# Kernel optimization log

Hardware: AMD Instinct MI355X
Metric: run time of the kernel (lower is better)

The kernel has to match this reference:

```python
import jax, jax.numpy as jnp
import numpy as np
import math

B, N, D = 4, 16384, 256
M, H = 64, 8
HD = D // H

def setup_inputs() -> dict:
    key = jax.random.key(0)
    ks = jax.random.split(key, 5)
    s = 1.0 / math.sqrt(D)
    return {
        "x": jax.random.normal(ks[0], (B, N, D), dtype=jnp.float32),
        "Ws": jax.random.normal(ks[1], (M, D), dtype=jnp.float32) * s,
        "bs": jnp.zeros((M,), dtype=jnp.float32),
        "Wqkv": jax.random.normal(ks[2], (3 * D, D), dtype=jnp.float32) * s,
        "Wo": jax.random.normal(ks[3], (D, D), dtype=jnp.float32) * s,
        "bo": jnp.zeros((D,), dtype=jnp.float32),
    }

def reference(x, Ws, bs, Wqkv, Wo, bo):
    # slice weights: softmax over N (dim=1), matching the torch code exactly
    logits = jnp.einsum('bnd,md->bnm', x, Ws) + bs          # [B,N,M]
    weights = jax.nn.softmax(logits, axis=1)                # softmax over N
    # pooling: tokens[b,m,d] = sum_n w[b,n,m] * x[b,n,d]
    tokens = jnp.einsum('bnm,bnd->bmd', weights, x)         # [B,M,D]
    # qkv projection (no bias)
    qkv = jnp.einsum('bmd,ed->bme', tokens, Wqkv)           # [B,M,3D]
    qkv = qkv.reshape(B, M, 3, H, HD)
    q = qkv[:, :, 0].transpose(0, 2, 1, 3)                  # [B,H,M,HD]
    k = qkv[:, :, 1].transpose(0, 2, 1, 3)
    v = qkv[:, :, 2].transpose(0, 2, 1, 3)
    scale = 1.0 / math.sqrt(HD)
    attn = jax.nn.softmax(jnp.einsum('bhmd,bhkd->bhmk', q, k) * scale, axis=-1)
    token_out = jnp.einsum('bhmk,bhkd->bhmd', attn, v)      # [B,H,M,HD]
    token_out = token_out.transpose(0, 2, 1, 3).reshape(B, M, D)
    token_out = jnp.einsum('bmd,ed->bme', token_out, Wo) + bo
    # unpooling: out[b,n,d] = sum_m w[b,n,m] * token_out[b,m,d]
    out = jnp.einsum('bnm,bmd->bnd', weights, token_out)    # [B,N,D]
    return out
```

## Files before the change

kernel.cpp:

```cpp
#include <hip/hip_runtime.h>
#include <math.h>

constexpr int B = 4;
constexpr int N = 16384;
constexpr int D = 256;
constexpr int M = 64;
constexpr int H = 8;

typedef __attribute__((ext_vector_type(8))) short short8;
typedef __attribute__((ext_vector_type(4))) float floatx4;

__device__ __forceinline__ float4 ld4(const float* p) {
  return *reinterpret_cast<const float4*>(p);
}
__device__ __forceinline__ void st4(float* p, float a, float b, float c, float d) {
  *reinterpret_cast<float4*>(p) = make_float4(a, b, c, d);
}
__device__ __forceinline__ unsigned short f2bf(float f) {
  unsigned u = __float_as_uint(f);
  unsigned r = (u + 0x7fffu + ((u >> 16) & 1u)) >> 16;
  return (unsigned short)r;
}

#define FMA16(acc, a4, b4)                       \
  do {                                           \
    acc[0][0] = fmaf(a4.x, b4.x, acc[0][0]);     \
    acc[0][1] = fmaf(a4.x, b4.y, acc[0][1]);     \
    acc[0][2] = fmaf(a4.x, b4.z, acc[0][2]);     \
    acc[0][3] = fmaf(a4.x, b4.w, acc[0][3]);     \
    acc[1][0] = fmaf(a4.y, b4.x, acc[1][0]);     \
    acc[1][1] = fmaf(a4.y, b4.y, acc[1][1]);     \
    acc[1][2] = fmaf(a4.y, b4.z, acc[1][2]);     \
    acc[1][3] = fmaf(a4.y, b4.w, acc[1][3]);     \
    acc[2][0] = fmaf(a4.z, b4.x, acc[2][0]);     \
    acc[2][1] = fmaf(a4.z, b4.y, acc[2][1]);     \
    acc[2][2] = fmaf(a4.z, b4.z, acc[2][2]);     \
    acc[2][3] = fmaf(a4.z, b4.w, acc[2][3]);     \
    acc[3][0] = fmaf(a4.w, b4.x, acc[3][0]);     \
    acc[3][1] = fmaf(a4.w, b4.y, acc[3][1]);     \
    acc[3][2] = fmaf(a4.w, b4.z, acc[3][2]);     \
    acc[3][3] = fmaf(a4.w, b4.w, acc[3][3]);     \
  } while (0)

__global__ __launch_bounds__(256) void k1_fused(
    const float* __restrict__ x, const float* __restrict__ Ws,
    const float* __restrict__ bs, unsigned short* __restrict__ xbT,
    unsigned short* __restrict__ En, unsigned short* __restrict__ Et,
    float* __restrict__ denom) {
  __shared__ unsigned short Xt[64][264];
  __shared__ unsigned short Wt[64][264];
  __shared__ unsigned short Es[64][72];
  __shared__ float red[64];
  const int b = blockIdx.y;
  const int n0 = blockIdx.x * 64;
  const int tid = threadIdx.x;
  const int w = tid >> 6, l = tid & 63;

#pragma unroll
  for (int p = 0; p < 16; ++p) {
    const int i = p * 256 + tid;
    const int row = i >> 6;
    const int c4 = (i & 63) * 4;
    float4 v = ld4(&x[((size_t)(b * N + n0 + row)) * D + c4]);
    unsigned u0 = (unsigned)f2bf(v.x) | ((unsigned)f2bf(v.y) << 16);
    unsigned u1 = (unsigned)f2bf(v.z) | ((unsigned)f2bf(v.w) << 16);
    *reinterpret_cast<uint2*>(&Xt[row][c4]) = make_uint2(u0, u1);
    float4 wv = ld4(&Ws[(size_t)row * D + c4]);
    unsigned w0 = (unsigned)f2bf(wv.x) | ((unsigned)f2bf(wv.y) << 16);
    unsigned w1 = (unsigned)f2bf(wv.z) | ((unsigned)f2bf(wv.w) << 16);
    *reinterpret_cast<uint2*>(&Wt[row][c4]) = make_uint2(w0, w1);
  }
  if (tid < 64) red[tid] = 0.0f;
  __syncthreads();

  floatx4 acc[4] = {{0.f, 0.f, 0.f, 0.f},
                    {0.f, 0.f, 0.f, 0.f},
                    {0.f, 0.f, 0.f, 0.f},
                    {0.f, 0.f, 0.f, 0.f}};
  const int ar = w * 16 + (l & 15);
  const int q8 = (l >> 4) * 8;
#pragma unroll
  for (int ks = 0; ks < 8; ++ks) {
    short8 a = *reinterpret_cast<short8*>(&Xt[ar][ks * 32 + q8]);
#pragma unroll
    for (int mt = 0; mt < 4; ++mt) {
      short8 bf = *reinterpret_cast<short8*>(&Wt[mt * 16 + (l & 15)][ks * 32 + q8]);
      acc[mt] = __builtin_amdgcn_mfma_f32_16x16x32_bf16(a, bf, acc[mt], 0, 0, 0);
    }
  }

  {
    const int t = tid;
#pragma unroll
    for (int g = 0; g < 4; ++g) {
      unsigned dw[8];
#pragma unroll
      for (int j = 0; j < 8; ++j) {
        const unsigned lo = Xt[g * 16 + 2 * j][t];
        const unsigned hi = Xt[g * 16 + 2 * j + 1][t];
        dw[j] = lo | (hi << 16);
      }
      const size_t base = ((size_t)(b * D + t)) * N + n0 + g * 16;
      *reinterpret_cast<uint4*>(&xbT[base]) =
          make_uint4(dw[0], dw[1], dw[2], dw[3]);
      *reinterpret_cast<uint4*>(&xbT[base + 8]) =
          make_uint4(dw[4], dw[5], dw[6], dw[7]);
    }
  }

#pragma unroll
  for (int mt = 0; mt < 4; ++mt) {
    const int m = mt * 16 + (l & 15);
    const float bsm = bs[m];
    float s = 0.0f;
#pragma unroll
    for (int r = 0; r < 4; ++r) {
      const int n = w * 16 + (l >> 4) * 4 + r;
      const float e = expf(acc[mt][r] + bsm);
      s += e;
      Es[n][m] = f2bf(e);
    }
    atomicAdd(&red[m], s);
  }
  __syncthreads();
  if (tid < 64) atomicAdd(&denom[b * M + tid], red[tid]);
#pragma unroll
  for (int p = 0; p < 2; ++p) {
    const int g = p * 256 + tid;
    const int n = g >> 3;
    const int m0 = (g & 7) * 8;
    short8 v = *reinterpret_cast<short8*>(&Es[n][m0]);
    *reinterpret_cast<short8*>(&En[((size_t)(b * N + n0 + n)) * M + m0]) = v;
  }
#pragma unroll
  for (int p = 0; p < 2; ++p) {
    const int g = p * 256 + tid;
    const int m = g >> 3;
    const int n8 = (g & 7) * 8;
    unsigned short bu[8];
#pragma unroll
    for (int k = 0; k < 8; ++k) bu[k] = Es[n8 + k][m];
    uint4 pk;
    pk.x = (unsigned)bu[0] | ((unsigned)bu[1] << 16);
    pk.y = (unsigned)bu[2] | ((unsigned)bu[3] << 16);
    pk.z = (unsigned)bu[4] | ((unsigned)bu[5] << 16);
    pk.w = (unsigned)bu[6] | ((unsigned)bu[7] << 16);
    *reinterpret_cast<uint4*>(&Et[((size_t)(b * M + m)) * N + n0 + n8]) = pk;
  }
}

__global__ __launch_bounds__(256) void k2_pool(
    const unsigned short* __restrict__ Et, const unsigned short* __restrict__ xbT,
    float* __restrict__ tokens) {
  __shared__ unsigned short EtS[64][72];
  __shared__ unsigned short XtS[64][72];
  const int dt = blockIdx.x, nc = blockIdx.y, b = blockIdx.z;
  const int d0 = dt * 64;
  const int tid = threadIdx.x;
  const int w = tid >> 6, l = tid & 63;
  floatx4 acc[4] = {{0.f, 0.f, 0.f, 0.f},
                    {0.f, 0.f, 0.f, 0.f},
                    {0.f, 0.f, 0.f, 0.f},
                    {0.f, 0.f, 0.f, 0.f}};
  const int q8 = (l >> 4) * 8;
  for (int kc = 0; kc < 8; ++kc) {
    const int nb = nc * 512 + kc * 64;
    __syncthreads();
#pragma unroll
    for (int p = 0; p < 2; ++p) {
      const int g = p * 256 + tid;
      const int row = g >> 3;
      const int c8 = (g & 7) * 8;
      *reinterpret_cast<short8*>(&EtS[row][c8]) =
          *reinterpret_cast<const short8*>(
              &Et[((size_t)(b * M + row)) * N + nb + c8]);
      *reinterpret_cast<short8*>(&XtS[row][c8]) =
          *reinterpret_cast<const short8*>(
              &xbT[((size_t)(b * D + d0 + row)) * N + nb + c8]);
    }
    __syncthreads();
#pragma unroll
    for (int ks = 0; ks < 2; ++ks) {
      short8 a = *reinterpret_cast<short8*>(&EtS[w * 16 + (l & 15)][ks * 32 + q8]);
#pragma unroll
      for (int dtile = 0; dtile < 4; ++dtile) {
        short8 bf = *reinterpret_cast<short8*>(
            &XtS[dtile * 16 + (l & 15)][ks * 32 + q8]);
        acc[dtile] =
            __builtin_amdgcn_mfma_f32_16x16x32_bf16(a, bf, acc[dtile], 0, 0, 0);
      }
    }
  }
#pragma unroll
  for (int dtile = 0; dtile < 4; ++dtile)
#pragma unroll
    for (int r = 0; r < 4; ++r) {
      const int m = w * 16 + (l >> 4) * 4 + r;
      const int d = d0 + dtile * 16 + (l & 15);
      atomicAdd(&tokens[((size_t)(b * M + m)) * D + d], acc[dtile][r]);
    }
}

__global__ __launch_bounds__(256) void k_proj(
    const float* __restrict__ A, const float* __restrict__ W,
    const float* __restrict__ bias, const float* __restrict__ denom,
    float* __restrict__ OutF, unsigned short* __restrict__ OutT, const int EC,
    const int mode) {
  __shared__ unsigned short At[64][264];
  __shared__ unsigned short Wt[64][264];
  __shared__ float Cs[64][68];
  const int et = blockIdx.x;
  const int b = blockIdx.y;
  const int tid = threadIdx.x;
  const int w = tid >> 6, l = tid & 63;
#pragma unroll
  for (int p = 0; p < 16; ++p) {
    const int i = p * 256 + tid;
    const int row = i >> 6;
    const int c4 = (i & 63) * 4;
    float4 av = ld4(&A[((size_t)(b * M + row)) * D + c4]);
    unsigned a0 = (unsigned)f2bf(av.x) | ((unsigned)f2bf(av.y) << 16);
    unsigned a1 = (unsigned)f2bf(av.z) | ((unsigned)f2bf(av.w) << 16);
    *reinterpret_cast<uint2*>(&At[row][c4]) = make_uint2(a0, a1);
    float4 wv = ld4(&W[((size_t)(et * 64 + row)) * D + c4]);
    unsigned w0 = (unsigned)f2bf(wv.x) | ((unsigned)f2bf(wv.y) << 16);
    unsigned w1 = (unsigned)f2bf(wv.z) | ((unsigned)f2bf(wv.w) << 16);
    *reinterpret_cast<uint2*>(&Wt[row][c4]) = make_uint2(w0, w1);
  }
  __syncthreads();
  floatx4 acc[4] = {{0.f, 0.f, 0.f, 0.f},
                    {0.f, 0.f, 0.f, 0.f},
                    {0.f, 0.f, 0.f, 0.f},
                    {0.f, 0.f, 0.f, 0.f}};
  const int ar = w * 16 + (l & 15);
  const int q8 = (l >> 4) * 8;
#pragma unroll
  for (int ks = 0; ks < 8; ++ks) {
    short8 a = *reinterpret_cast<short8*>(&At[ar][ks * 32 + q8]);
#pragma unroll
    for (int mt = 0; mt < 4; ++mt) {
      short8 bf = *reinterpret_cast<short8*>(&Wt[mt * 16 + (l & 15)][ks * 32 + q8]);
      acc[mt] = __builtin_amdgcn_mfma_f32_16x16x32_bf16(a, bf, acc[mt], 0, 0, 0);
    }
  }
  if (mode == 0) {
#pragma unroll
    for (int mt = 0; mt < 4; ++mt) {
#pragma unroll
      for (int r = 0; r < 4; ++r) {
        const int row = w * 16 + (l >> 4) * 4 + r;
        const float rcp = 1.0f / denom[b * M + row];
        const int e = et * 64 + mt * 16 + (l & 15);
        OutF[((size_t)(b * M + row)) * EC + e] = acc[mt][r] * rcp;
      }
    }
  } else {
#pragma unroll
    for (int mt = 0; mt < 4; ++mt) {
#pragma unroll
      for (int r = 0; r < 4; ++r) {
        const int row = w * 16 + (l >> 4) * 4 + r;
        const float rcp = 1.0f / denom[b * M + row];
        const int el = mt * 16 + (l & 15);
        const float bv = bias[et * 64 + el];
        Cs[row][el] = (acc[mt][r] + bv) * rcp;
      }
    }
    __syncthreads();
#pragma unroll
    for (int p = 0; p < 2; ++p) {
      const int g = p * 256 + tid;
      const int e = g >> 3;
      const int m0 = (g & 7) * 8;
      unsigned short bu[8];
#pragma unroll
      for (int k = 0; k < 8; ++k) bu[k] = f2bf(Cs[m0 + k][e]);
      uint4 pk;
      pk.x = (unsigned)bu[0] | ((unsigned)bu[1] << 16);
      pk.y = (unsigned)bu[2] | ((unsigned)bu[3] << 16);
      pk.z = (unsigned)bu[4] | ((unsigned)bu[5] << 16);
      pk.w = (unsigned)bu[6] | ((unsigned)bu[7] << 16);
      *reinterpret_cast<uint4*>(
          &OutT[((size_t)(b * D + et * 64 + e)) * M + m0]) = pk;
    }
  }
}

__global__ __launch_bounds__(256) void k4_attn(
    const float* __restrict__ qkv, float* __restrict__ attn_o) {
  __shared__ float qt[32][68];
  __shared__ float kt[32][68];
  __shared__ float vv[64][36];
  __shared__ float P[64][68];
  const int b = blockIdx.x >> 3;
  const int h = blockIdx.x & 7;
  const int tid = threadIdx.x;
  for (int i = tid; i < 512; i += 256) {
    const int m = i >> 3;
    const int c4 = (i & 7) * 4;
    const float* base = &qkv[((size_t)(b * M + m)) * 768 + h * 32 + c4];
    float4 q4 = ld4(base);
    float4 k4 = ld4(base + 256);
    float4 v4 = ld4(base + 512);
    qt[c4 + 0][m] = q4.x; qt[c4 + 1][m] = q4.y; qt[c4 + 2][m] = q4.z; qt[c4 + 3][m] = q4.w;
    kt[c4 + 0][m] = k4.x; kt[c4 + 1][m] = k4.y; kt[c4 + 2][m] = k4.z; kt[c4 + 3][m] = k4.w;
    *reinterpret_cast<float4*>(&vv[m][c4]) = v4;
  }
  __syncthreads();
  {
    const int tm4 = (tid & 15) * 4;
    const int tn4 = (tid >> 4) * 4;
    float acc[4][4] = {};
    for (int k = 0; k < 32; ++k) {
      float4 a4 = ld4(&qt[k][tn4]);
      float4 b4 = ld4(&kt[k][tm4]);
      FMA16(acc, a4, b4);
    }
    const float scale = 0.17677669529663687f;
#pragma unroll
    for (int i = 0; i < 4; ++i)
      st4(&P[tn4 + i][tm4], acc[i][0] * scale, acc[i][1] * scale,
          acc[i][2] * scale, acc[i][3] * scale);
  }
  __syncthreads();
  if (tid < 64) {
    float mx = -1e30f;
    for (int j = 0; j < 64; ++j) mx = fmaxf(mx, P[tid][j]);
    float s = 0.0f;
    for (int j = 0; j < 64; ++j) {
      const float e = expf(P[tid][j] - mx);
      P[tid][j] = e;
      s += e;
    }
    const float r = 1.0f / s;
    for (int j = 0; j < 64; ++j) P[tid][j] *= r;
  }
  __syncthreads();
  if (tid < 128) {
    const int i0 = (tid >> 3) * 4;
    const int c0 = (tid & 7) * 4;
    float o[4][4] = {};
    for (int j = 0; j < 64; ++j) {
      float4 v4 = ld4(&vv[j][c0]);
#pragma unroll
      for (int ii = 0; ii < 4; ++ii) {
        const float p = P[i0 + ii][j];
        o[ii][0] = fmaf(p, v4.x, o[ii][0]);
        o[ii][1] = fmaf(p, v4.y, o[ii][1]);
        o[ii][2] = fmaf(p, v4.z, o[ii][2]);
        o[ii][3] = fmaf(p, v4.w, o[ii][3]);
      }
    }
#pragma unroll
    for (int ii = 0; ii < 4; ++ii)
      st4(&attn_o[((size_t)(b * M + i0 + ii)) * D + h * 32 + c0],
          o[ii][0], o[ii][1], o[ii][2], o[ii][3]);
  }
}

__global__ __launch_bounds__(256) void k6_unpool(
    const unsigned short* __restrict__ En, const unsigned short* __restrict__ TpT,
    float* __restrict__ out) {
  __shared__ unsigned short EnS[64][72];
  __shared__ unsigned short TpS[64][72];
  const int dt = blockIdx.x, nt = blockIdx.y, b = blockIdx.z;
  const int n0 = nt * 64, d0 = dt * 64;
  const int tid = threadIdx.x;
  const int w = tid >> 6, l = tid & 63;
#pragma unroll
  for (int p = 0; p < 2; ++p) {
    const int g = p * 256 + tid;
    const int row = g >> 3;
    const int c8 = (g & 7) * 8;
    *reinterpret_cast<short8*>(&EnS[row][c8]) =
        *reinterpret_cast<const short8*>(
            &En[((size_t)(b * N + n0 + row)) * M + c8]);
    *reinterpret_cast<short8*>(&TpS[row][c8]) =
        *reinterpret_cast<const short8*>(
            &TpT[((size_t)(b * D + d0 + row)) * M + c8]);
  }
  __syncthreads();
  floatx4 acc[4] = {{0.f, 0.f, 0.f, 0.f},
                    {0.f, 0.f, 0.f, 0.f},
                    {0.f, 0.f, 0.f, 0.f},
                    {0.f, 0.f, 0.f, 0.f}};
  const int q8 = (l >> 4) * 8;
#pragma unroll
  for (int ks = 0; ks < 2; ++ks) {
    short8 a = *reinterpret_cast<short8*>(&EnS[w * 16 + (l & 15)][ks * 32 + q8]);
#pragma unroll
    for (int dtile = 0; dtile < 4; ++dtile) {
      short8 bf = *reinterpret_cast<short8*>(
          &TpS[dtile * 16 + (l & 15)][ks * 32 + q8]);
      acc[dtile] =
          __builtin_amdgcn_mfma_f32_16x16x32_bf16(a, bf, acc[dtile], 0, 0, 0);
    }
  }
#pragma unroll
  for (int dtile = 0; dtile < 4; ++dtile)
#pragma unroll
    for (int r = 0; r < 4; ++r) {
      const int n = n0 + w * 16 + (l >> 4) * 4 + r;
      const int d = d0 + dtile * 16 + (l & 15);
      out[((size_t)(b * N + n)) * D + d] = acc[dtile][r];
    }
}

extern "C" void kernel_launch(void* const* d_in, const int* in_sizes, int n_in,
                              void* d_out, int out_size, void* d_ws,
                              size_t ws_size, hipStream_t stream) {
  const float* x = (const float*)d_in[0];
  const float* Ws = (const float*)d_in[1];
  const float* bs = (const float*)d_in[2];
  const float* Wqkv = (const float*)d_in[3];
  const float* Wo = (const float*)d_in[4];
  const float* bo = (const float*)d_in[5];
  float* out = (float*)d_out;

  char* p = (char*)d_ws;
  unsigned short* xbT = (unsigned short*)p;      p += (size_t)B * N * D * 2;
  unsigned short* En = (unsigned short*)p;       p += (size_t)B * N * M * 2;
  unsigned short* Et = (unsigned short*)p;       p += (size_t)B * N * M * 2;
  unsigned short* TpT = (unsigned short*)p;      p += (size_t)B * D * M * 2;
  float* denom = (float*)p;                      p += (size_t)B * M * 4;
  float* tokens = (float*)p;                     p += (size_t)B * M * D * 4;
  float* qkv = (float*)p;                        p += (size_t)B * M * 3 * D * 4;
  float* attn_o = (float*)p;                     p += (size_t)B * M * D * 4;

  hipMemsetAsync(denom, 0, (size_t)B * M * sizeof(float), stream);
  hipMemsetAsync(tokens, 0, (size_t)B * M * D * sizeof(float), stream);

  k1_fused<<<dim3(N / 64, B), 256, 0, stream>>>(x, Ws, bs, xbT, En, Et, denom);
  k2_pool<<<dim3(D / 64, N / 512, B), 256, 0, stream>>>(Et, xbT, tokens);
  k_proj<<<dim3(12, B), 256, 0, stream>>>(tokens, Wqkv, nullptr, denom, qkv,
                                          nullptr, 768, 0);
  k4_attn<<<dim3(B * H), 256, 0, stream>>>(qkv, attn_o);
  k_proj<<<dim3(4, B), 256, 0, stream>>>(attn_o, Wo, bo, denom, nullptr, TpT,
                                         256, 1);
  k6_unpool<<<dim3(D / 64, N / 64, B), 256, 0, stream>>>(En, TpT, out);
}
```

Before: 190.7 us.

## Replace padded LDS tiles with XOR-swizzled layouts and split k1 staging into K-chunks

All LDS tiles drop row padding and use an XOR swizzle on 8-element groups, aiming to avoid bank conflicts on the short8 MFMA fragment loads while using less shared memory. k1 now stages x and Ws in two 128-column chunks with a sync per chunk, which halves its LDS footprint and may raise occupancy. The transposed xbT write is reorganised per chunk, with each thread writing 32 contiguous n values. The transpose reads of single shorts through the swizzle may still conflict, and the extra barriers add some sync cost.

```diff
diff --git a/kernel.cpp b/kernel.cpp
--- a/kernel.cpp
+++ b/kernel.cpp
@@ -20,6 +20,16 @@
   unsigned u = __float_as_uint(f);
   unsigned r = (u + 0x7fffu + ((u >> 16) & 1u)) >> 16;
   return (unsigned short)r;
+}
+
+__device__ __forceinline__ int swz128(int r, int c) {
+  return r * 128 + ((((c >> 3) ^ (r & 7)) << 3) | (c & 7));
+}
+__device__ __forceinline__ int swz64(int r, int c) {
+  return r * 64 + ((((c >> 3) ^ (r & 7)) << 3) | (c & 7));
+}
+__device__ __forceinline__ int swz256(int r, int c) {
+  return r * 256 + ((((c >> 3) ^ (r & 7)) << 3) | (c & 7));
 }
 
 #define FMA16(acc, a4, b4)                       \
@@ -47,65 +57,72 @@
     const float* __restrict__ bs, unsigned short* __restrict__ xbT,
     unsigned short* __restrict__ En, unsigned short* __restrict__ Et,
     float* __restrict__ denom) {
-  __shared__ unsigned short Xt[64][264];
-  __shared__ unsigned short Wt[64][264];
-  __shared__ unsigned short Es[64][72];
+  __shared__ unsigned short Xt[64 * 128];
+  __shared__ unsigned short Wt[64 * 128];
+  __shared__ unsigned short Es[64 * 64];
   __shared__ float red[64];
   const int b = blockIdx.y;
   const int n0 = blockIdx.x * 64;
   const int tid = threadIdx.x;
   const int w = tid >> 6, l = tid & 63;
-
-#pragma unroll
-  for (int p = 0; p < 16; ++p) {
-    const int i = p * 256 + tid;
-    const int row = i >> 6;
-    const int c4 = (i & 63) * 4;
-    float4 v = ld4(&x[((size_t)(b * N + n0 + row)) * D + c4]);
-    unsigned u0 = (unsigned)f2bf(v.x) | ((unsigned)f2bf(v.y) << 16);
-    unsigned u1 = (unsigned)f2bf(v.z) | ((unsigned)f2bf(v.w) << 16);
-    *reinterpret_cast<uint2*>(&Xt[row][c4]) = make_uint2(u0, u1);
-    float4 wv = ld4(&Ws[(size_t)row * D + c4]);
-    unsigned w0 = (unsigned)f2bf(wv.x) | ((unsigned)f2bf(wv.y) << 16);
-    unsigned w1 = (unsigned)f2bf(wv.z) | ((unsigned)f2bf(wv.w) << 16);
-    *reinterpret_cast<uint2*>(&Wt[row][c4]) = make_uint2(w0, w1);
-  }
+  const int q = l >> 4, q8 = q * 8;
+  const int ar = w * 16 + (l & 15);
+
   if (tid < 64) red[tid] = 0.0f;
-  __syncthreads();
 
   floatx4 acc[4] = {{0.f, 0.f, 0.f, 0.f},
                     {0.f, 0.f, 0.f, 0.f},
                     {0.f, 0.f, 0.f, 0.f},
                     {0.f, 0.f, 0.f, 0.f}};
-  const int ar = w * 16 + (l & 15);
-  const int q8 = (l >> 4) * 8;
-#pragma unroll
-  for (int ks = 0; ks < 8; ++ks) {
-    short8 a = *reinterpret_cast<short8*>(&Xt[ar][ks * 32 + q8]);
-#pragma unroll
-    for (int mt = 0; mt < 4; ++mt) {
-      short8 bf = *reinterpret_cast<short8*>(&Wt[mt * 16 + (l & 15)][ks * 32 + q8]);
-      acc[mt] = __builtin_amdgcn_mfma_f32_16x16x32_bf16(a, bf, acc[mt], 0, 0, 0);
-    }
-  }
-
-  {
-    const int t = tid;
-#pragma unroll
-    for (int g = 0; g < 4; ++g) {
-      unsigned dw[8];
-#pragma unroll
-      for (int j = 0; j < 8; ++j) {
-        const unsigned lo = Xt[g * 16 + 2 * j][t];
-        const unsigned hi = Xt[g * 16 + 2 * j + 1][t];
+
+  for (int kc = 0; kc < 2; ++kc) {
+#pragma unroll
+    for (int p = 0; p < 8; ++p) {
+      const int idx = p * 256 + tid;
+      const int row = idx >> 5;
+      const int c4 = (idx & 31) * 4;
+      float4 v = ld4(&x[((size_t)(b * N + n0 + row)) * D + kc * 128 + c4]);
+      unsigned u0 = (unsigned)f2bf(v.x) | ((unsigned)f2bf(v.y) << 16);
+      unsigned u1 = (unsigned)f2bf(v.z) | ((unsigned)f2bf(v.w) << 16);
+      *reinterpret_cast<uint2*>(&Xt[swz128(row, c4)]) = make_uint2(u0, u1);
+      float4 wv = ld4(&Ws[(size_t)row * D + kc * 128 + c4]);
+      unsigned w0 = (unsigned)f2bf(wv.x) | ((unsigned)f2bf(wv.y) << 16);
+      unsigned w1 = (unsigned)f2bf(wv.z) | ((unsigned)f2bf(wv.w) << 16);
+      *reinterpret_cast<uint2*>(&Wt[swz128(row, c4)]) = make_uint2(w0, w1);
+    }
+    __syncthreads();
+#pragma unroll
+    for (int ks = 0; ks < 4; ++ks) {
+      short8 a = *reinterpret_cast<short8*>(&Xt[swz128(ar, ks * 32 + q8)]);
+#pragma unroll
+      for (int mt = 0; mt < 4; ++mt) {
+        short8 bf = *reinterpret_cast<short8*>(
+            &Wt[swz128(mt * 16 + (l & 15), ks * 32 + q8)]);
+        acc[mt] =
+            __builtin_amdgcn_mfma_f32_16x16x32_bf16(a, bf, acc[mt], 0, 0, 0);
+      }
+    }
+    {
+      const int dc = tid >> 1;
+      const int nh = (tid & 1) * 32;
+      unsigned dw[16];
+#pragma unroll
+      for (int j = 0; j < 16; ++j) {
+        const unsigned lo = Xt[swz64(0, 0) * 0 + swz128(nh + 2 * j, dc)];
+        const unsigned hi = Xt[swz128(nh + 2 * j + 1, dc)];
         dw[j] = lo | (hi << 16);
       }
-      const size_t base = ((size_t)(b * D + t)) * N + n0 + g * 16;
+      const size_t base = ((size_t)(b * D + kc * 128 + dc)) * N + n0 + nh;
       *reinterpret_cast<uint4*>(&xbT[base]) =
           make_uint4(dw[0], dw[1], dw[2], dw[3]);
       *reinterpret_cast<uint4*>(&xbT[base + 8]) =
           make_uint4(dw[4], dw[5], dw[6], dw[7]);
-    }
+      *reinterpret_cast<uint4*>(&xbT[base + 16]) =
+          make_uint4(dw[8], dw[9], dw[10], dw[11]);
+      *reinterpret_cast<uint4*>(&xbT[base + 24]) =
+          make_uint4(dw[12], dw[13], dw[14], dw[15]);
+    }
+    __syncthreads();
   }
 
 #pragma unroll
@@ -115,10 +132,10 @@
     float s = 0.0f;
 #pragma unroll
     for (int r = 0; r < 4; ++r) {
-      const int n = w * 16 + (l >> 4) * 4 + r;
+      const int n = w * 16 + q * 4 + r;
       const float e = expf(acc[mt][r] + bsm);
       s += e;
-      Es[n][m] = f2bf(e);
+      Es[swz64(n, m)] = f2bf(e);
     }
     atomicAdd(&red[m], s);
   }
@@ -129,7 +146,7 @@
     const int g = p * 256 + tid;
     const int n = g >> 3;
     const int m0 = (g & 7) * 8;
-    short8 v = *reinterpret_cast<short8*>(&Es[n][m0]);
+    short8 v = *reinterpret_cast<short8*>(&Es[swz64(n, m0)]);
     *reinterpret_cast<short8*>(&En[((size_t)(b * N + n0 + n)) * M + m0]) = v;
   }
 #pragma unroll
@@ -139,7 +156,7 @@
     const int n8 = (g & 7) * 8;
     unsigned short bu[8];
 #pragma unroll
-    for (int k = 0; k < 8; ++k) bu[k] = Es[n8 + k][m];
+    for (int k = 0; k < 8; ++k) bu[k] = Es[swz64(n8 + k, m)];
     uint4 pk;
     pk.x = (unsigned)bu[0] | ((unsigned)bu[1] << 16);
     pk.y = (unsigned)bu[2] | ((unsigned)bu[3] << 16);
@@ -152,8 +169,8 @@
 __global__ __launch_bounds__(256) void k2_pool(
     const unsigned short* __restrict__ Et, const unsigned short* __restrict__ xbT,
     float* __restrict__ tokens) {
-  __shared__ unsigned short EtS[64][72];
-  __shared__ unsigned short XtS[64][72];
+  __shared__ unsigned short EtS[64 * 64];
+  __shared__ unsigned short XtS[64 * 64];
   const int dt = blockIdx.x, nc = blockIdx.y, b = blockIdx.z;
   const int d0 = dt * 64;
   const int tid = threadIdx.x;
@@ -171,21 +188,22 @@
       const int g = p * 256 + tid;
       const int row = g >> 3;
       const int c8 = (g & 7) * 8;
-      *reinterpret_cast<short8*>(&EtS[row][c8]) =
+      *reinterpret_cast<short8*>(&EtS[swz64(row, c8)]) =
           *reinterpret_cast<const short8*>(
               &Et[((size_t)(b * M + row)) * N + nb + c8]);
-      *reinterpret_cast<short8*>(&XtS[row][c8]) =
+      *reinterpret_cast<short8*>(&XtS[swz64(row, c8)]) =
           *reinterpret_cast<const short8*>(
               &xbT[((size_t)(b * D + d0 + row)) * N + nb + c8]);
     }
     __syncthreads();
 #pragma unroll
     for (int ks = 0; ks < 2; ++ks) {
-      short8 a = *reinterpret_cast<short8*>(&EtS[w * 16 + (l & 15)][ks * 32 + q8]);
+      short8 a = *reinterpret_cast<short8*>(
+          &EtS[swz64(w * 16 + (l & 15), ks * 32 + q8)]);
 #pragma unroll
       for (int dtile = 0; dtile < 4; ++dtile) {
         short8 bf = *reinterpret_cast<short8*>(
-            &XtS[dtile * 16 + (l & 15)][ks * 32 + q8]);
+            &XtS[swz64(dtile * 16 + (l & 15), ks * 32 + q8)]);
         acc[dtile] =
             __builtin_amdgcn_mfma_f32_16x16x32_bf16(a, bf, acc[dtile], 0, 0, 0);
       }
@@ -206,13 +224,14 @@
     const float* __restrict__ bias, const float* __restrict__ denom,
     float* __restrict__ OutF, unsigned short* __restrict__ OutT, const int EC,
     const int mode) {
-  __shared__ unsigned short At[64][264];
-  __shared__ unsigned short Wt[64][264];
+  __shared__ unsigned short At[64 * 256];
+  __shared__ unsigned short Wt[64 * 256];
   __shared__ float Cs[64][68];
   const int et = blockIdx.x;
   const int b = blockIdx.y;
   const int tid = threadIdx.x;
   const int w = tid >> 6, l = tid & 63;
+  const int q8 = (l >> 4) * 8;
 #pragma unroll
   for (int p = 0; p < 16; ++p) {
     const int i = p * 256 + tid;
@@ -221,11 +240,11 @@
     float4 av = ld4(&A[((size_t)(b * M + row)) * D + c4]);
     unsigned a0 = (unsigned)f2bf(av.x) | ((unsigned)f2bf(av.y) << 16);
     unsigned a1 = (unsigned)f2bf(av.z) | ((unsigned)f2bf(av.w) << 16);
-    *reinterpret_cast<uint2*>(&At[row][c4]) = make_uint2(a0, a1);
+    *reinterpret_cast<uint2*>(&At[swz256(row, c4)]) = make_uint2(a0, a1);
     float4 wv = ld4(&W[((size_t)(et * 64 + row)) * D + c4]);
     unsigned w0 = (unsigned)f2bf(wv.x) | ((unsigned)f2bf(wv.y) << 16);
     unsigned w1 = (unsigned)f2bf(wv.z) | ((unsigned)f2bf(wv.w) << 16);
-    *reinterpret_cast<uint2*>(&Wt[row][c4]) = make_uint2(w0, w1);
+    *reinterpret_cast<uint2*>(&Wt[swz256(row, c4)]) = make_uint2(w0, w1);
   }
   __syncthreads();
   floatx4 acc[4] = {{0.f, 0.f, 0.f, 0.f},
@@ -233,13 +252,13 @@
                     {0.f, 0.f, 0.f, 0.f},
                     {0.f, 0.f, 0.f, 0.f}};
   const int ar = w * 16 + (l & 15);
-  const int q8 = (l >> 4) * 8;
 #pragma unroll
   for (int ks = 0; ks < 8; ++ks) {
-    short8 a = *reinterpret_cast<short8*>(&At[ar][ks * 32 + q8]);
+    short8 a = *reinterpret_cast<short8*>(&At[swz256(ar, ks * 32 + q8)]);
 #pragma unroll
     for (int mt = 0; mt < 4; ++mt) {
-      short8 bf = *reinterpret_cast<short8*>(&Wt[mt * 16 + (l & 15)][ks * 32 + q8]);
+      short8 bf = *reinterpret_cast<short8*>(
+          &Wt[swz256(mt * 16 + (l & 15), ks * 32 + q8)]);
       acc[mt] = __builtin_amdgcn_mfma_f32_16x16x32_bf16(a, bf, acc[mt], 0, 0, 0);
     }
   }
@@ -361,8 +380,8 @@
 __global__ __launch_bounds__(256) void k6_unpool(
     const unsigned short* __restrict__ En, const unsigned short* __restrict__ TpT,
     float* __restrict__ out) {
-  __shared__ unsigned short EnS[64][72];
-  __shared__ unsigned short TpS[64][72];
+  __shared__ unsigned short EnS[64 * 64];
+  __shared__ unsigned short TpS[64 * 64];
   const int dt = blockIdx.x, nt = blockIdx.y, b = blockIdx.z;
   const int n0 = nt * 64, d0 = dt * 64;
   const int tid = threadIdx.x;
@@ -372,10 +391,10 @@
     const int g = p * 256 + tid;
     const int row = g >> 3;
     const int c8 = (g & 7) * 8;
-    *reinterpret_cast<short8*>(&EnS[row][c8]) =
+    *reinterpret_cast<short8*>(&EnS[swz64(row, c8)]) =
         *reinterpret_cast<const short8*>(
             &En[((size_t)(b * N + n0 + row)) * M + c8]);
-    *reinterpret_cast<short8*>(&TpS[row][c8]) =
+    *reinterpret_cast<short8*>(&TpS[swz64(row, c8)]) =
         *reinterpret_cast<const short8*>(
             &TpT[((size_t)(b * D + d0 + row)) * M + c8]);
   }
@@ -387,11 +406,12 @@
   const int q8 = (l >> 4) * 8;
 #pragma unroll
   for (int ks = 0; ks < 2; ++ks) {
-    short8 a = *reinterpret_cast<short8*>(&EnS[w * 16 + (l & 15)][ks * 32 + q8]);
+    short8 a = *reinterpret_cast<short8*>(
+        &EnS[swz64(w * 16 + (l & 15), ks * 32 + q8)]);
 #pragma unroll
     for (int dtile = 0; dtile < 4; ++dtile) {
       short8 bf = *reinterpret_cast<short8*>(
-          &TpS[dtile * 16 + (l & 15)][ks * 32 + q8]);
+          &TpS[swz64(dtile * 16 + (l & 15), ks * 32 + q8)]);
       acc[dtile] =
           __builtin_amdgcn_mfma_f32_16x16x32_bf16(a, bf, acc[dtile], 0, 0, 0);
     }
```

Measured after the change: 216.0 us. 1.13x slower.

## Pre-convert Ws to bf16, halve k1 tile, tile xbT/Et layout for pool

Applied to the files above, without the earlier changes.

Adds a small kernel that converts Ws to bf16 once, so each k1 block no longer reloads and converts the whole fp32 weight matrix into shared memory; k1 instead reads the bf16 weights straight from global. k1 now handles 32 tokens per block with an XOR-swizzled shared tile, which cuts LDS use and doubles the block count. The transposed xbT and Et buffers are stored in 64-token tiles so that k2_pool reads contiguous chunks. This trades redundant weight conversion for uncached global B-operand loads in the MFMA loop and one extra launch.

```diff
diff --git a/kernel.cpp b/kernel.cpp
--- a/kernel.cpp
+++ b/kernel.cpp
@@ -20,6 +20,10 @@
   unsigned u = __float_as_uint(f);
   unsigned r = (u + 0x7fffu + ((u >> 16) & 1u)) >> 16;
   return (unsigned short)r;
+}
+
+__device__ __forceinline__ int swz256(int r, int c) {
+  return r * 256 + ((((c >> 3) ^ (r & 7)) << 3) | (c & 7));
 }
 
 #define FMA16(acc, a4, b4)                       \
@@ -42,110 +46,115 @@
     acc[3][3] = fmaf(a4.w, b4.w, acc[3][3]);     \
   } while (0)
 
+__global__ __launch_bounds__(256) void kws_cvt(const float* __restrict__ Ws,
+                                               unsigned short* __restrict__ Wsb) {
+  const int i = blockIdx.x * 256 + threadIdx.x;
+  float4 v = ld4(&Ws[(size_t)i * 4]);
+  unsigned u0 = (unsigned)f2bf(v.x) | ((unsigned)f2bf(v.y) << 16);
+  unsigned u1 = (unsigned)f2bf(v.z) | ((unsigned)f2bf(v.w) << 16);
+  *reinterpret_cast<uint2*>(&Wsb[(size_t)i * 4]) = make_uint2(u0, u1);
+}
+
 __global__ __launch_bounds__(256) void k1_fused(
-    const float* __restrict__ x, const float* __restrict__ Ws,
+    const float* __restrict__ x, const unsigned short* __restrict__ Wsb,
     const float* __restrict__ bs, unsigned short* __restrict__ xbT,
     unsigned short* __restrict__ En, unsigned short* __restrict__ Et,
     float* __restrict__ denom) {
-  __shared__ unsigned short Xt[64][264];
-  __shared__ unsigned short Wt[64][264];
-  __shared__ unsigned short Es[64][72];
+  __shared__ unsigned short Xt[32 * 256];
+  __shared__ unsigned short Es[32 * 64];
   __shared__ float red[64];
   const int b = blockIdx.y;
-  const int n0 = blockIdx.x * 64;
+  const int n0 = blockIdx.x * 32;
+  const int tile = n0 >> 6;
+  const int half = n0 & 32;
   const int tid = threadIdx.x;
   const int w = tid >> 6, l = tid & 63;
-
-#pragma unroll
-  for (int p = 0; p < 16; ++p) {
-    const int i = p * 256 + tid;
-    const int row = i >> 6;
-    const int c4 = (i & 63) * 4;
+  const int q = l >> 4, q8 = q * 8;
+  const int wn = (w & 1) * 16;
+  const int mt0 = (w >> 1) * 2;
+
+  if (tid < 64) red[tid] = 0.0f;
+
+#pragma unroll
+  for (int p = 0; p < 8; ++p) {
+    const int idx = p * 256 + tid;
+    const int row = idx >> 6;
+    const int c4 = (idx & 63) * 4;
     float4 v = ld4(&x[((size_t)(b * N + n0 + row)) * D + c4]);
     unsigned u0 = (unsigned)f2bf(v.x) | ((unsigned)f2bf(v.y) << 16);
     unsigned u1 = (unsigned)f2bf(v.z) | ((unsigned)f2bf(v.w) << 16);
-    *reinterpret_cast<uint2*>(&Xt[row][c4]) = make_uint2(u0, u1);
-    float4 wv = ld4(&Ws[(size_t)row * D + c4]);
-    unsigned w0 = (unsigned)f2bf(wv.x) | ((unsigned)f2bf(wv.y) << 16);
-    unsigned w1 = (unsigned)f2bf(wv.z) | ((unsigned)f2bf(wv.w) << 16);
-    *reinterpret_cast<uint2*>(&Wt[row][c4]) = make_uint2(w0, w1);
-  }
-  if (tid < 64) red[tid] = 0.0f;
-  __syncthreads();
-
-  floatx4 acc[4] = {{0.f, 0.f, 0.f, 0.f},
-                    {0.f, 0.f, 0.f, 0.f},
-                    {0.f, 0.f, 0.f, 0.f},
-                    {0.f, 0.f, 0.f, 0.f}};
-  const int ar = w * 16 + (l & 15);
-  const int q8 = (l >> 4) * 8;
+    *reinterpret_cast<uint2*>(&Xt[swz256(row, c4)]) = make_uint2(u0, u1);
+  }
+  __syncthreads();
+
+  floatx4 acc0 = {0.f, 0.f, 0.f, 0.f};
+  floatx4 acc1 = {0.f, 0.f, 0.f, 0.f};
+  const int ar = wn + (l & 15);
+  const int br0 = (mt0 * 16 + (l & 15)) * 256;
+  const int br1 = ((mt0 + 1) * 16 + (l & 15)) * 256;
 #pragma unroll
   for (int ks = 0; ks < 8; ++ks) {
-    short8 a = *reinterpret_cast<short8*>(&Xt[ar][ks * 32 + q8]);
-#pragma unroll
-    for (int mt = 0; mt < 4; ++mt) {
-      short8 bf = *reinterpret_cast<short8*>(&Wt[mt * 16 + (l & 15)][ks * 32 + q8]);
-      acc[mt] = __builtin_amdgcn_mfma_f32_16x16x32_bf16(a, bf, acc[mt], 0, 0, 0);
-    }
+    short8 a = *reinterpret_cast<short8*>(&Xt[swz256(ar, ks * 32 + q8)]);
+    short8 b0 = *reinterpret_cast<const short8*>(&Wsb[br0 + ks * 32 + q8]);
+    short8 b1 = *reinterpret_cast<const short8*>(&Wsb[br1 + ks * 32 + q8]);
+    acc0 = __builtin_amdgcn_mfma_f32_16x16x32_bf16(a, b0, acc0, 0, 0, 0);
+    acc1 = __builtin_amdgcn_mfma_f32_16x16x32_bf16(a, b1, acc1, 0, 0, 0);
   }
 
   {
-    const int t = tid;
-#pragma unroll
-    for (int g = 0; g < 4; ++g) {
-      unsigned dw[8];
-#pragma unroll
-      for (int j = 0; j < 8; ++j) {
-        const unsigned lo = Xt[g * 16 + 2 * j][t];
-        const unsigned hi = Xt[g * 16 + 2 * j + 1][t];
-        dw[j] = lo | (hi << 16);
-      }
-      const size_t base = ((size_t)(b * D + t)) * N + n0 + g * 16;
-      *reinterpret_cast<uint4*>(&xbT[base]) =
-          make_uint4(dw[0], dw[1], dw[2], dw[3]);
-      *reinterpret_cast<uint4*>(&xbT[base + 8]) =
-          make_uint4(dw[4], dw[5], dw[6], dw[7]);
-    }
-  }
-
-#pragma unroll
-  for (int mt = 0; mt < 4; ++mt) {
-    const int m = mt * 16 + (l & 15);
-    const float bsm = bs[m];
-    float s = 0.0f;
+    unsigned dw[16];
+#pragma unroll
+    for (int j = 0; j < 16; ++j) {
+      const unsigned lo = Xt[swz256(2 * j, tid)];
+      const unsigned hi = Xt[swz256(2 * j + 1, tid)];
+      dw[j] = lo | (hi << 16);
+    }
+    const size_t base = (((size_t)(b * (N / 64) + tile)) * D + tid) * 64 + half;
+    *reinterpret_cast<uint4*>(&xbT[base]) = make_uint4(dw[0], dw[1], dw[2], dw[3]);
+    *reinterpret_cast<uint4*>(&xbT[base + 8]) = make_uint4(dw[4], dw[5], dw[6], dw[7]);
+    *reinterpret_cast<uint4*>(&xbT[base + 16]) = make_uint4(dw[8], dw[9], dw[10], dw[11]);
+    *reinterpret_cast<uint4*>(&xbT[base + 24]) = make_uint4(dw[12], dw[13], dw[14], dw[15]);
+  }
+
+  {
+    const float bs0 = bs[mt0 * 16 + (l & 15)];
+    const float bs1 = bs[(mt0 + 1) * 16 + (l & 15)];
+    float s0 = 0.f, s1 = 0.f;
 #pragma unroll
     for (int r = 0; r < 4; ++r) {
-      const int n = w * 16 + (l >> 4) * 4 + r;
-      const float e = expf(acc[mt][r] + bsm);
-      s += e;
-      Es[n][m] = f2bf(e);
-    }
-    atomicAdd(&red[m], s);
+      const int n = wn + q * 4 + r;
+      const float e0 = expf(acc0[r] + bs0);
+      const float e1 = expf(acc1[r] + bs1);
+      s0 += e0;
+      s1 += e1;
+      Es[n * 64 + mt0 * 16 + (l & 15)] = f2bf(e0);
+      Es[n * 64 + (mt0 + 1) * 16 + (l & 15)] = f2bf(e1);
+    }
+    atomicAdd(&red[mt0 * 16 + (l & 15)], s0);
+    atomicAdd(&red[(mt0 + 1) * 16 + (l & 15)], s1);
   }
   __syncthreads();
   if (tid < 64) atomicAdd(&denom[b * M + tid], red[tid]);
-#pragma unroll
-  for (int p = 0; p < 2; ++p) {
-    const int g = p * 256 + tid;
-    const int n = g >> 3;
-    const int m0 = (g & 7) * 8;
-    short8 v = *reinterpret_cast<short8*>(&Es[n][m0]);
+
+  {
+    short8 v = *reinterpret_cast<short8*>(&Es[tid * 8]);
+    const int n = tid >> 3, m0 = (tid & 7) * 8;
     *reinterpret_cast<short8*>(&En[((size_t)(b * N + n0 + n)) * M + m0]) = v;
   }
-#pragma unroll
-  for (int p = 0; p < 2; ++p) {
-    const int g = p * 256 + tid;
-    const int m = g >> 3;
-    const int n8 = (g & 7) * 8;
+  {
+    const int m = tid >> 2;
+    const int n8 = (tid & 3) * 8;
     unsigned short bu[8];
 #pragma unroll
-    for (int k = 0; k < 8; ++k) bu[k] = Es[n8 + k][m];
+    for (int k = 0; k < 8; ++k) bu[k] = Es[(n8 + k) * 64 + m];
     uint4 pk;
     pk.x = (unsigned)bu[0] | ((unsigned)bu[1] << 16);
     pk.y = (unsigned)bu[2] | ((unsigned)bu[3] << 16);
     pk.z = (unsigned)bu[4] | ((unsigned)bu[5] << 16);
     pk.w = (unsigned)bu[6] | ((unsigned)bu[7] << 16);
-    *reinterpret_cast<uint4*>(&Et[((size_t)(b * M + m)) * N + n0 + n8]) = pk;
+    const size_t base =
+        (((size_t)(b * (N / 64) + tile)) * M + m) * 64 + half + n8;
+    *reinterpret_cast<uint4*>(&Et[base]) = pk;
   }
 }
 
@@ -164,7 +173,7 @@
                     {0.f, 0.f, 0.f, 0.f}};
   const int q8 = (l >> 4) * 8;
   for (int kc = 0; kc < 8; ++kc) {
-    const int nb = nc * 512 + kc * 64;
+    const int tIdx = nc * 8 + kc;
     __syncthreads();
 #pragma unroll
     for (int p = 0; p < 2; ++p) {
@@ -173,10 +182,10 @@
       const int c8 = (g & 7) * 8;
       *reinterpret_cast<short8*>(&EtS[row][c8]) =
           *reinterpret_cast<const short8*>(
-              &Et[((size_t)(b * M + row)) * N + nb + c8]);
+              &Et[(((size_t)(b * (N / 64) + tIdx)) * M + row) * 64 + c8]);
       *reinterpret_cast<short8*>(&XtS[row][c8]) =
           *reinterpret_cast<const short8*>(
-              &xbT[((size_t)(b * D + d0 + row)) * N + nb + c8]);
+              &xbT[(((size_t)(b * (N / 64) + tIdx)) * D + d0 + row) * 64 + c8]);
     }
     __syncthreads();
 #pragma unroll
@@ -213,6 +222,7 @@
   const int b = blockIdx.y;
   const int tid = threadIdx.x;
   const int w = tid >> 6, l = tid & 63;
+  const int q8 = (l >> 4) * 8;
 #pragma unroll
   for (int p = 0; p < 16; ++p) {
     const int i = p * 256 + tid;
@@ -233,7 +243,6 @@
                     {0.f, 0.f, 0.f, 0.f},
                     {0.f, 0.f, 0.f, 0.f}};
   const int ar = w * 16 + (l & 15);
-  const int q8 = (l >> 4) * 8;
 #pragma unroll
   for (int ks = 0; ks < 8; ++ks) {
     short8 a = *reinterpret_cast<short8*>(&At[ar][ks * 32 + q8]);
@@ -422,6 +431,7 @@
   unsigned short* En = (unsigned short*)p;       p += (size_t)B * N * M * 2;
   unsigned short* Et = (unsigned short*)p;       p += (size_t)B * N * M * 2;
   unsigned short* TpT = (unsigned short*)p;      p += (size_t)B * D * M * 2;
+  unsigned short* Wsb = (unsigned short*)p;      p += (size_t)M * D * 2;
   float* denom = (float*)p;                      p += (size_t)B * M * 4;
   float* tokens = (float*)p;                     p += (size_t)B * M * D * 4;
   float* qkv = (float*)p;                        p += (size_t)B * M * 3 * D * 4;
@@ -430,7 +440,8 @@
   hipMemsetAsync(denom, 0, (size_t)B * M * sizeof(float), stream);
   hipMemsetAsync(tokens, 0, (size_t)B * M * D * sizeof(float), stream);
 
-  k1_fused<<<dim3(N / 64, B), 256, 0, stream>>>(x, Ws, bs, xbT, En, Et, denom);
+  kws_cvt<<<dim3(16), 256, 0, stream>>>(Ws, Wsb);
+  k1_fused<<<dim3(N / 32, B), 256, 0, stream>>>(x, Wsb, bs, xbT, En, Et, denom);
   k2_pool<<<dim3(D / 64, N / 512, B), 256, 0, stream>>>(Et, xbT, tokens);
   k_proj<<<dim3(12, B), 256, 0, stream>>>(tokens, Wqkv, nullptr, denom, qkv,
                                           nullptr, 768, 0);
```

New measurement: 207.3 us. 1.09x slower.
